# Kernel optimization log

Measured on AMD Instinct MI355X. Metric: run time of the kernel, lower is better.

## Reference

```python
import jax, jax.numpy as jnp
import numpy as np

BATCH, T, C = 32, 600, 64
DEPTH = 2            # logsig depth 2 -> [increments, Levy areas]
N_SEGMENTS = 50
N_HIDDENS = 512
LOGSIG_CH = C + C * (C - 1) // 2   # 2080, Lyndon-word count at depth 2
IN_SIZE = C + LOGSIG_CH            # 2144 = logsig + start point


def _t_vec(nT, n_segments):
    # matches: [int(round(x)) for x in np.linspace(1, nT, n_segments+1)]
    return np.asarray([int(round(v)) for v in np.linspace(1, nT, n_segments + 1)])


def setup_inputs() -> dict:
    key = jax.random.key(0)
    k0, k1, k2, k3, k4 = jax.random.split(key, 5)
    x = jax.random.normal(k0, (BATCH, T, C), jnp.float32)
    s = 1.0 / np.sqrt(N_HIDDENS)
    w_ih = jax.random.uniform(k1, (4 * N_HIDDENS, IN_SIZE), jnp.float32, -s, s)
    w_hh = jax.random.uniform(k2, (4 * N_HIDDENS, N_HIDDENS), jnp.float32, -s, s)
    b_ih = jax.random.uniform(k3, (4 * N_HIDDENS,), jnp.float32, -s, s)
    b_hh = jax.random.uniform(k4, (4 * N_HIDDENS,), jnp.float32, -s, s)
    return {"x": x, "w_ih": w_ih, "w_hh": w_hh, "b_ih": b_ih, "b_hh": b_hh}


def _logsig_and_start(x):
    """Depth-2 segmented log-signature + segment start points.
    Returns (logsig (B,S,LOGSIG_CH), start (B,S,C))."""
    B, nT, c = x.shape
    tv = _t_vec(nT, N_SEGMENTS)
    starts = tv[:-1] - 1               # segment start frame indices
    ends = tv[1:] - 1                  # segment end frame indices
    # step s (between frames s and s+1) belongs to segment i iff tv[i]-1 <= s < tv[i+1]-1
    step_ids = jnp.asarray(np.searchsorted(tv[1:] - 1, np.arange(nT - 1), side='right'))
    dx = x[:, 1:] - x[:, :-1]                            # (B, T-1, C)
    # per-step outer product x_{t-} (X) dx_t, then segmented sum over steps
    prod = jnp.einsum('btc,btd->btcd', x[:, :-1], dx)    # (B, T-1, C, C)
    Q = jax.ops.segment_sum(jnp.moveaxis(prod, 1, 0), step_ids,
                            num_segments=N_SEGMENTS)      # (S, B, C, C)
    xa = x[:, starts]                                    # (B, S, C)
    xb = x[:, ends]
    inc = xb - xa                                        # level-1 logsig
    # shift origin to segment start: P = sum (X_rel (X) dX)
    P = jnp.moveaxis(Q, 0, 1) - jnp.einsum('bsc,bsd->bscd', xa, inc)
    A = 0.5 * (P - jnp.swapaxes(P, -1, -2))              # Levy area (antisym)
    iu, ju = np.triu_indices(c, 1)                       # Lyndon words (i,j), i<j, lex order
    logsig = jnp.concatenate([inc, A[:, :, iu, ju]], axis=-1)
    return logsig, xa


def _lstm(feats, w_ih, w_hh, b_ih, b_hh):
    B = feats.shape[0]
    H = N_HIDDENS
    gx = jnp.einsum('bsf,gf->bsg', feats, w_ih) + b_ih + b_hh  # (B,S,4H)

    def step(carry, g_t):
        h, cc = carry
        g = g_t + h @ w_hh.T
        i, f, gg, o = jnp.split(g, 4, axis=-1)
        i = jax.nn.sigmoid(i); f = jax.nn.sigmoid(f)
        gg = jnp.tanh(gg); o = jax.nn.sigmoid(o)
        cc = f * cc + i * gg
        h = o * jnp.tanh(cc)
        return (h, cc), h

    h0 = jnp.zeros((B, H), feats.dtype)
    (_, _), hs = jax.lax.scan(step, (h0, h0), jnp.moveaxis(gx, 1, 0))
    return jnp.moveaxis(hs, 0, 1)                        # (B, S, H)


def reference(x, w_ih, w_hh, b_ih, b_hh):
    logsig, x_sp = _logsig_and_start(x)
    feats = jnp.concatenate([logsig, x_sp], axis=-1)      # (B, S, IN_SIZE)
    return _lstm(feats, w_ih, w_hh, b_ih, b_hh)
```

## Files before the change

### kernel.cpp

```cpp
#include <hip/hip_runtime.h>
#include <math.h>

typedef _Float16 f16;
typedef _Float16 f16x8 __attribute__((ext_vector_type(8)));
typedef _Float16 f16x4 __attribute__((ext_vector_type(4)));
typedef float    f32x4 __attribute__((ext_vector_type(4)));

#define BATCH 32
#define TT    600
#define CC    64
#define SEG   50
#define HH    512
#define G4    2048
#define FF    2144
#define MM    1600
#define MP    1664
#define NPAIR 2016
#define CVB   512
#define WRK   208
#define SLOT16 16384
#define KT    67
#define BUFB  12288

struct TV { int v[51]; };

__device__ __forceinline__ void async_copy16(char* lds, const char* g) {
  __builtin_amdgcn_global_load_lds(
      (const __attribute__((address_space(1))) unsigned int*)g,
      (__attribute__((address_space(3))) unsigned int*)lds, 16, 0, 0);
}

__device__ __forceinline__ float sigm(float x) { return 1.f / (1.f + __expf(-x)); }
__device__ __forceinline__ float tanh_(float x) {
  float ax = fabsf(x);
  float e  = __expf(2.f * ax);
  float t  = 1.f - 2.f / (e + 1.f);
  return x < 0.f ? -t : t;
}
__device__ __forceinline__ unsigned short f16_bits(f16 v) {
  union { f16 f; unsigned short u; } c; c.f = v; return c.u;
}
__device__ __forceinline__ unsigned int f32_bits(float v) {
  union { float f; unsigned int u; } c; c.f = v; return c.u;
}

__global__ void prep_kernel(const float* __restrict__ x, f16* __restrict__ fhi, TV tv,
                            const float4* __restrict__ w_ih, const float4* __restrict__ w_hh,
                            f16x4* __restrict__ w16, f16x4* __restrict__ whh16,
                            unsigned int* __restrict__ ready) {
  __shared__ float xs[13 * CC];
  int m   = blockIdx.x;
  int tid = threadIdx.x;

  if (m >= MP) {
    int cb   = m - MP;
    int gtid = cb * 256 + tid;
    int nth  = CVB * 256;
    for (int i = gtid; i < G4 * FF / 4; i += nth) {
      float4 v = w_ih[i];
      f16x4 o = {(f16)v.x, (f16)v.y, (f16)v.z, (f16)v.w};
      w16[i] = o;
    }
    for (int i = gtid; i < G4 * HH / 4; i += nth) {
      float4 v = w_hh[i];
      f16x4 o = {(f16)v.x, (f16)v.y, (f16)v.z, (f16)v.w};
      whh16[i] = o;
    }
    if (cb == 0)
      for (int i = tid; i < 544; i += 256) ready[i] = 0u;
    return;
  }

  f16* rhi = fhi + (size_t)m * FF;
  if (m >= MM) {
    unsigned int* a = (unsigned int*)rhi;
    for (int i = tid; i < FF / 2; i += 256) a[i] = 0u;
    return;
  }
  int bb = m & 31, ss = m >> 5;
  int t0 = tv.v[ss] - 1, t1 = tv.v[ss + 1] - 1;
  int len = t1 - t0;
  for (int i = tid; i < (len + 1) * CC; i += 256)
    xs[i] = x[(size_t)bb * TT * CC + (size_t)(t0 + (i >> 6)) * CC + (i & 63)];
  __syncthreads();

  if (tid < CC) {
    float xa  = xs[tid];
    float inc = xs[len * CC + tid] - xa;
    rhi[tid] = (f16)inc;
    rhi[2080 + tid] = (f16)xa;
  }

  int p0 = tid * 8;
  if (p0 < NPAIR) {
    int c = 0, rem = p0;
    while (rem >= 63 - c) { rem -= 63 - c; c++; }
    int d = c + 1 + rem;
    int cs[8], dd[8];
#pragma unroll
    for (int i = 0; i < 8; i++) {
      cs[i] = c; dd[i] = d;
      d++; if (d == 64) { c++; d = c + 1; }
    }
    float acc[8], xc[8], xd[8];
#pragma unroll
    for (int i = 0; i < 8; i++) { acc[i] = 0.f; xc[i] = xs[cs[i]]; xd[i] = xs[dd[i]]; }
    for (int t = 1; t <= len; t++) {
#pragma unroll
      for (int i = 0; i < 8; i++) {
        float nc = xs[t * CC + cs[i]], nd = xs[t * CC + dd[i]];
        acc[i] += xc[i] * (nd - xd[i]) - xd[i] * (nc - xc[i]);
        xc[i] = nc; xd[i] = nd;
      }
    }
#pragma unroll
    for (int i = 0; i < 8; i++) {
      int ci = cs[i], di = dd[i];
      float xac = xs[ci], xad = xs[di];
      float incc = xs[len * CC + ci] - xac, incd = xs[len * CC + di] - xad;
      float v = 0.5f * acc[i] - 0.5f * (xac * incd - xad * incc);
      rhi[64 + p0 + i] = (f16)v;
    }
  }
}

__global__ __launch_bounds__(256) void fused_kernel(
    const f16* __restrict__ fhi, const f16* __restrict__ w16,
    const float* __restrict__ bih, const float* __restrict__ bhh,
    const f16* __restrict__ whh16, float* __restrict__ gx,
    unsigned short* __restrict__ hbuf, unsigned int* __restrict__ ready,
    unsigned int* __restrict__ gxcnt, float* __restrict__ out) {
  __shared__ __align__(16) char smem[61440];
  int tid  = threadIdx.x;
  int lane = tid & 63;

  if (blockIdx.x >= 32) {
    int w  = blockIdx.x - 32;
    int wn = tid >> 6;
    int rowq = tid >> 2;
    int colq = (tid & 3) * 8;
    int ldst = tid * 16;
    int quad16 = (lane >> 4) * 16;
    int am = lane & 15;
    unsigned int* gxa = (unsigned int*)gx;

    for (int t = 0; t < 2; t++) {
      int id = w + t * WRK;
      int mt = id >> 4, nt = id & 15;
      int m0 = mt * 64, n0 = nt * 128;

      const f16* pa  = fhi + (size_t)(m0 + rowq) * FF + colq;
      const f16* pb0 = w16 + (size_t)(n0 + rowq) * FF + colq;
      const f16* pb1 = pb0 + (size_t)64 * FF;

      f32x4 zero4 = {0.f, 0.f, 0.f, 0.f};
      f32x4 acc[4][2];
#pragma unroll
      for (int i = 0; i < 4; i++) { acc[i][0] = zero4; acc[i][1] = zero4; }

      for (int kp = 0; kp < 3; kp++) {
        char* b = smem + kp * BUFB;
        int koff = kp * 32;
        async_copy16(b + ldst,        (const char*)(pa + koff));
        async_copy16(b + 4096 + ldst, (const char*)(pb0 + koff));
        async_copy16(b + 8192 + ldst, (const char*)(pb1 + koff));
      }

      for (int kt = 0; kt < KT; kt++) {
        if (kt + 3 < KT) {
          char* b = smem + ((kt + 3) % 5) * BUFB;
          int koff = (kt + 3) * 32;
          async_copy16(b + ldst,        (const char*)(pa + koff));
          async_copy16(b + 4096 + ldst, (const char*)(pb0 + koff));
          async_copy16(b + 8192 + ldst, (const char*)(pb1 + koff));
          asm volatile("s_waitcnt vmcnt(9)" ::: "memory");
        } else if (kt + 3 == KT) {
          asm volatile("s_waitcnt vmcnt(6)" ::: "memory");
        } else if (kt + 2 == KT) {
          asm volatile("s_waitcnt vmcnt(3)" ::: "memory");
        } else {
          asm volatile("s_waitcnt vmcnt(0)" ::: "memory");
        }
        __builtin_amdgcn_s_barrier();
        __builtin_amdgcn_sched_barrier(0);

        char* bb   = smem + (kt % 5) * BUFB;
        char* ldsA = bb;
        char* ldsB = bb + 4096;
        f16x8 bfr[2];
#pragma unroll
        for (int ni = 0; ni < 2; ni++)
          bfr[ni] = *(const f16x8*)(ldsB + (wn * 32 + ni * 16 + am) * 64 + quad16);
#pragma unroll
        for (int mi = 0; mi < 4; mi++) {
          f16x8 ah = *(const f16x8*)(ldsA + (mi * 16 + am) * 64 + quad16);
#pragma unroll
          for (int ni = 0; ni < 2; ni++)
            acc[mi][ni] = __builtin_amdgcn_mfma_f32_16x16x32_f16(ah, bfr[ni], acc[mi][ni], 0, 0, 0);
        }
      }

#pragma unroll
      for (int ni = 0; ni < 2; ni++) {
        int ncol = n0 + wn * 32 + ni * 16 + (lane & 15);
        float bv = bih[ncol] + bhh[ncol];
#pragma unroll
        for (int mi = 0; mi < 4; mi++) {
          int mrow = m0 + mi * 16 + (lane >> 4) * 4;
#pragma unroll
          for (int r = 0; r < 4; r++)
            __hip_atomic_store(gxa + (size_t)(mrow + r) * G4 + ncol,
                               f32_bits(acc[mi][ni][r] + bv),
                               __ATOMIC_RELAXED, __HIP_MEMORY_SCOPE_AGENT);
        }
      }
      __syncthreads();
      if (tid == 0)
        __hip_atomic_fetch_add(&gxcnt[mt], 1u, __ATOMIC_RELAXED,
                               __HIP_MEMORY_SCOPE_AGENT);
    }
    return;
  }

  f16* hs = (f16*)smem;
  float* gb = (float*)(smem + 32768);

  int gate = tid >> 6;
  int u0   = blockIdx.x * 16;
  int wg   = blockIdx.x;

  f16x8 bf[16];
  {
    const f16* wrow = whh16 + (size_t)(gate * HH + u0 + (lane & 15)) * HH + (lane >> 4) * 8;
#pragma unroll
    for (int ks = 0; ks < 16; ks++) bf[ks] = *(const f16x8*)(wrow + ks * 32);
  }

  int b1 = tid >> 4;
  int ul = tid & 15;
  float cst0 = 0.f, cst1 = 0.f;
  int aq  = (lane >> 4);
  int am  = (lane & 15);
  int col = lane & 15;
  int rbase = (lane >> 4) * 4;

  for (int s = 0; s < SEG; s++) {
    if ((s & 1) == 0) {
      if (tid == 0) {
        while (__hip_atomic_load(&gxcnt[s >> 1], __ATOMIC_RELAXED,
                                 __HIP_MEMORY_SCOPE_AGENT) < 16u)
          __builtin_amdgcn_s_sleep(1);
      }
      __syncthreads();
    }

    float gxr0[4], gxr1[4];
#pragma unroll
    for (int r = 0; r < 4; r++) {
      int b = rbase + r;
      gxr0[r] = gx[(size_t)((s << 5) + b) * G4 + gate * HH + u0 + col];
      gxr1[r] = gx[(size_t)((s << 5) + b + 16) * G4 + gate * HH + u0 + col];
    }

    f32x4 acc0 = {0.f, 0.f, 0.f, 0.f};
    f32x4 acc1 = {0.f, 0.f, 0.f, 0.f};

    if (s > 0) {
      unsigned int tgt = (unsigned int)s;
      if (tid < 32) {
        while (__hip_atomic_load(&ready[tid * 16], __ATOMIC_RELAXED,
                                 __HIP_MEMORY_SCOPE_AGENT) < tgt)
          __builtin_amdgcn_s_sleep(1);
      }
      __syncthreads();

      const char* hrd = (const char*)(hbuf + (size_t)s * SLOT16);
#pragma unroll
      for (int c = 0; c < 8; c++)
        async_copy16((char*)hs + c * 4096 + tid * 16, hrd + c * 4096 + tid * 16);
      __syncthreads();

#pragma unroll
      for (int ks = 0; ks < 16; ks++) {
        f16x8 a0 = *(const f16x8*)((char*)hs + (((ks * 4 + aq) * 32) + am) * 16);
        f16x8 a1 = *(const f16x8*)((char*)hs + (((ks * 4 + aq) * 32) + 16 + am) * 16);
        acc0 = __builtin_amdgcn_mfma_f32_16x16x32_f16(a0, bf[ks], acc0, 0, 0, 0);
        acc1 = __builtin_amdgcn_mfma_f32_16x16x32_f16(a1, bf[ks], acc1, 0, 0, 0);
      }
    }

#pragma unroll
    for (int r = 0; r < 4; r++) {
      int b = rbase + r;
      gb[(gate * 32 + b) * 16 + col]      = acc0[r] + gxr0[r];
      gb[(gate * 32 + b + 16) * 16 + col] = acc1[r] + gxr1[r];
    }
    __syncthreads();

    unsigned short* hwr = hbuf + (size_t)(s + 1) * SLOT16;
    int k = u0 + ul;
    float h0, h1;
    {
      float i_ = sigm(gb[(0 * 32 + b1) * 16 + ul]), f_ = sigm(gb[(1 * 32 + b1) * 16 + ul]);
      float g_ = tanh_(gb[(2 * 32 + b1) * 16 + ul]), o_ = sigm(gb[(3 * 32 + b1) * 16 + ul]);
      cst0 = f_ * cst0 + i_ * g_;
      h0 = o_ * tanh_(cst0);
    }
    {
      int b2 = b1 + 16;
      float i_ = sigm(gb[(0 * 32 + b2) * 16 + ul]), f_ = sigm(gb[(1 * 32 + b2) * 16 + ul]);
      float g_ = tanh_(gb[(2 * 32 + b2) * 16 + ul]), o_ = sigm(gb[(3 * 32 + b2) * 16 + ul]);
      cst1 = f_ * cst1 + i_ * g_;
      h1 = o_ * tanh_(cst1);
    }

    if (s < SEG - 1) {
      __hip_atomic_store(hwr + ((k >> 3) * 32 + b1) * 8 + (k & 7),
                         f16_bits((f16)h0), __ATOMIC_RELAXED, __HIP_MEMORY_SCOPE_AGENT);
      __hip_atomic_store(hwr + ((k >> 3) * 32 + (b1 + 16)) * 8 + (k & 7),
                         f16_bits((f16)h1), __ATOMIC_RELAXED, __HIP_MEMORY_SCOPE_AGENT);
      __syncthreads();
      if (tid == 0)
        __hip_atomic_store(&ready[wg * 16], (unsigned int)(s + 1),
                           __ATOMIC_RELAXED, __HIP_MEMORY_SCOPE_AGENT);
    }

    out[(size_t)(b1 * SEG + s) * HH + k] = h0;
    out[(size_t)((b1 + 16) * SEG + s) * HH + k] = h1;
  }
}

extern "C" void kernel_launch(void* const* d_in, const int* in_sizes, int n_in,
                              void* d_out, int out_size, void* d_ws, size_t ws_size,
                              hipStream_t stream) {
  const float* x    = (const float*)d_in[0];
  const float* w_ih = (const float*)d_in[1];
  const float* w_hh = (const float*)d_in[2];
  const float* b_ih = (const float*)d_in[3];
  const float* b_hh = (const float*)d_in[4];
  float* out = (float*)d_out;

  char* ws = (char*)d_ws;
  f16*   fhi   = (f16*)(ws + 0);
  f16*   w16   = (f16*)(ws + 7135232);
  f16*   whh16 = (f16*)(ws + 15921152);
  float* gx    = (float*)(ws + 18018304);
  unsigned short* hbuf  = (unsigned short*)(ws + 31649792);
  unsigned int*   ready = (unsigned int*)(ws + 33288192);

  TV tv;
  double step = 599.0 / 50.0;
  for (int i = 0; i <= 50; i++) {
    double v = (double)i * step + 1.0;
    tv.v[i] = (int)nearbyint(v);
  }
  tv.v[50] = 600;

  unsigned int* gxcnt = ready + 512;

  prep_kernel<<<dim3(MP + CVB), dim3(256), 0, stream>>>(
      x, fhi, tv, (const float4*)w_ih, (const float4*)w_hh,
      (f16x4*)w16, (f16x4*)whh16, ready);

  fused_kernel<<<dim3(32 + WRK), dim3(256), 0, stream>>>(
      fhi, w16, b_ih, b_hh, whh16, gx, hbuf, ready, gxcnt, out);
}
```

Before: 245.1 us.

## Swizzle GEMM LDS layout and make LSTM waits per-wave without block barriers

The input-projection GEMM now XOR-swizzles the 16-byte k-chunks in shared memory on both the async copy and the fragment reads, meant to remove LDS bank conflicts. The LSTM recurrent loop replaces the single-thread spin plus __syncthreads with every wave polling the ready flags and the gx counter and agreeing through __all. The hidden-state async copy is now issued before the gx loads so it overlaps them. This removes one or two block-wide barriers per step but adds redundant polling traffic from every wave. Correctness relies on each wave seeing the flags before reading data without a block barrier.

```diff
diff --git a/kernel.cpp b/kernel.cpp
--- a/kernel.cpp
+++ b/kernel.cpp
@@ -138,19 +138,32 @@
     int w  = blockIdx.x - 32;
     int wn = tid >> 6;
     int rowq = tid >> 2;
-    int colq = (tid & 3) * 8;
     int ldst = tid * 16;
-    int quad16 = (lane >> 4) * 16;
-    int am = lane & 15;
+    int quad = lane >> 4;
+    int am   = lane & 15;
     unsigned int* gxa = (unsigned int*)gx;
+
+    int qsrc = ((tid & 3) ^ ((tid >> 3) & 3)) * 8;
+
+    int offA[4], offB[2];
+#pragma unroll
+    for (int mi = 0; mi < 4; mi++) {
+      int ra = mi * 16 + am;
+      offA[mi] = ra * 64 + ((quad ^ ((ra >> 1) & 3)) * 16);
+    }
+#pragma unroll
+    for (int ni = 0; ni < 2; ni++) {
+      int rb = wn * 32 + ni * 16 + am;
+      offB[ni] = 4096 + rb * 64 + ((quad ^ ((rb >> 1) & 3)) * 16);
+    }
 
     for (int t = 0; t < 2; t++) {
       int id = w + t * WRK;
       int mt = id >> 4, nt = id & 15;
       int m0 = mt * 64, n0 = nt * 128;
 
-      const f16* pa  = fhi + (size_t)(m0 + rowq) * FF + colq;
-      const f16* pb0 = w16 + (size_t)(n0 + rowq) * FF + colq;
+      const f16* pa  = fhi + (size_t)(m0 + rowq) * FF + qsrc;
+      const f16* pb0 = w16 + (size_t)(n0 + rowq) * FF + qsrc;
       const f16* pb1 = pb0 + (size_t)64 * FF;
 
       f32x4 zero4 = {0.f, 0.f, 0.f, 0.f};
@@ -184,16 +197,13 @@
         __builtin_amdgcn_s_barrier();
         __builtin_amdgcn_sched_barrier(0);
 
-        char* bb   = smem + (kt % 5) * BUFB;
-        char* ldsA = bb;
-        char* ldsB = bb + 4096;
+        char* bb = smem + (kt % 5) * BUFB;
         f16x8 bfr[2];
-#pragma unroll
-        for (int ni = 0; ni < 2; ni++)
-          bfr[ni] = *(const f16x8*)(ldsB + (wn * 32 + ni * 16 + am) * 64 + quad16);
+        bfr[0] = *(const f16x8*)(bb + offB[0]);
+        bfr[1] = *(const f16x8*)(bb + offB[1]);
 #pragma unroll
         for (int mi = 0; mi < 4; mi++) {
-          f16x8 ah = *(const f16x8*)(ldsA + (mi * 16 + am) * 64 + quad16);
+          f16x8 ah = *(const f16x8*)(bb + offA[mi]);
 #pragma unroll
           for (int ni = 0; ni < 2; ni++)
             acc[mi][ni] = __builtin_amdgcn_mfma_f32_16x16x32_f16(ah, bfr[ni], acc[mi][ni], 0, 0, 0);
@@ -245,13 +255,29 @@
   int rbase = (lane >> 4) * 4;
 
   for (int s = 0; s < SEG; s++) {
-    if ((s & 1) == 0) {
-      if (tid == 0) {
-        while (__hip_atomic_load(&gxcnt[s >> 1], __ATOMIC_RELAXED,
-                                 __HIP_MEMORY_SCOPE_AGENT) < 16u)
-          __builtin_amdgcn_s_sleep(1);
-      }
-      __syncthreads();
+    {
+      unsigned tgt = (unsigned)s;
+      int mt = s >> 1;
+      bool needg = ((s & 1) == 0);
+      for (;;) {
+        bool ok = true;
+        if (s > 0)
+          ok = __hip_atomic_load(&ready[(lane & 31) * 16], __ATOMIC_RELAXED,
+                                 __HIP_MEMORY_SCOPE_AGENT) >= tgt;
+        if (needg)
+          ok = ok && (__hip_atomic_load(&gxcnt[mt], __ATOMIC_RELAXED,
+                                        __HIP_MEMORY_SCOPE_AGENT) >= 16u);
+        if (__all(ok)) break;
+        __builtin_amdgcn_s_sleep(1);
+      }
+      asm volatile("" ::: "memory");
+    }
+
+    if (s > 0) {
+      const char* hrd = (const char*)(hbuf + (size_t)s * SLOT16);
+#pragma unroll
+      for (int c = 0; c < 8; c++)
+        async_copy16((char*)hs + c * 4096 + tid * 16, hrd + c * 4096 + tid * 16);
     }
 
     float gxr0[4], gxr1[4];
@@ -266,18 +292,6 @@
     f32x4 acc1 = {0.f, 0.f, 0.f, 0.f};
 
     if (s > 0) {
-      unsigned int tgt = (unsigned int)s;
-      if (tid < 32) {
-        while (__hip_atomic_load(&ready[tid * 16], __ATOMIC_RELAXED,
-                                 __HIP_MEMORY_SCOPE_AGENT) < tgt)
-          __builtin_amdgcn_s_sleep(1);
-      }
-      __syncthreads();
-
-      const char* hrd = (const char*)(hbuf + (size_t)s * SLOT16);
-#pragma unroll
-      for (int c = 0; c < 8; c++)
-        async_copy16((char*)hs + c * 4096 + tid * 16, hrd + c * 4096 + tid * 16);
       __syncthreads();
 
 #pragma unroll
```

Result: slower. 262.3 us (+7.0%).
